# Optimization experiments

Measured on AMD Instinct MI355X. Metric: run time of the kernel, lower is better.

Reference implementation:

```python
import jax, jax.numpy as jnp
import numpy as np

N_NODES = 50000
N_EDGES = 800000
SD = 128
N_GRAPHS = 128
HL = 4
VOCAB = 1340
N_CLASSES = 41
BN_EPS = 1e-5


def setup_inputs() -> dict:
    key = jax.random.key(0)
    ks = jax.random.split(key, 20)
    s = 1.0 / np.sqrt(SD)
    inp = {
        "node_ids": jax.random.randint(ks[0], (N_NODES,), 0, VOCAB),
        "edge_index": jax.random.randint(ks[1], (2, N_EDGES), 0, N_NODES),
        "batch": jnp.sort(jax.random.randint(ks[2], (N_NODES,), 0, N_GRAPHS)),
        "emb": jax.random.normal(ks[3], (VOCAB, SD)) * 0.05,
        "in_W1": jax.random.normal(ks[4], (SD, SD)) * s,
        "in_b1": jnp.zeros((SD,)),
        "in_W2": jax.random.normal(ks[5], (SD, SD)) * s,
        "in_b2": jnp.zeros((SD,)),
        "bn_gamma": jnp.ones((SD,)),
        "bn_beta": jnp.zeros((SD,)),
        "bn_mean": jnp.zeros((SD,)),
        "bn_var": jnp.ones((SD,)),
        "out_W1": jax.random.normal(ks[6], (SD, SD)) * s,
        "out_b1": jnp.zeros((SD,)),
        "out_W2": jax.random.normal(ks[7], (SD, SD)) * s,
        "out_b2": jnp.zeros((SD,)),
        "fc1_W": jax.random.normal(ks[8], (SD, SD)) * s,
        "fc1_b": jnp.zeros((SD,)),
        "fc2_W": jax.random.normal(ks[9], (N_CLASSES, SD)) * s,
        "fc2_b": jnp.zeros((N_CLASSES,)),
    }
    return inp


def reference(node_ids, edge_index, batch, emb, in_W1, in_b1, in_W2, in_b2,
              bn_gamma, bn_beta, bn_mean, bn_var,
              out_W1, out_b1, out_W2, out_b2, fc1_W, fc1_b, fc2_W, fc2_b):
    src, dst = edge_index[0], edge_index[1]

    def gin(x, W1, b1, W2, b2):
        # GINConv with eps=0: mlp(x + sum_{j in N(i)} x_j)
        agg = jax.ops.segment_sum(x[src], dst, num_segments=N_NODES)
        h = x + agg
        h = jnp.maximum(h @ W1.T + b1, 0.0)
        return h @ W2.T + b2

    def bn(x):
        # eval-mode BatchNorm1d with running stats
        return (x - bn_mean) * (bn_gamma / jnp.sqrt(bn_var + BN_EPS)) + bn_beta

    x = emb[node_ids]  # [N, SD]
    x = bn(jnp.maximum(gin(x, in_W1, in_b1, in_W2, in_b2), 0.0))
    for _ in range(HL):  # shared weights, repeated hl times
        x = bn(jnp.maximum(gin(x, in_W1, in_b1, in_W2, in_b2), 0.0))
    x = jnp.maximum(gin(x, out_W1, out_b1, out_W2, out_b2), 0.0)
    pooled = jax.ops.segment_sum(x, batch, num_segments=N_GRAPHS)  # [G, SD]
    h = jnp.maximum(pooled @ fc1_W.T + fc1_b, 0.0)
    return h @ fc2_W.T + fc2_b  # [G, 41]
```

## Files before the change

kernel.cpp:

```cpp
#include <hip/hip_runtime.h>

#define NN 50000
#define NE 800000
#define NG 128
#define NC 41
#define CAP 64
#define XG 8
#define RNG 6250

typedef __attribute__((ext_vector_type(8))) short bfrag8;
typedef __attribute__((ext_vector_type(4))) float facc4;

__device__ __forceinline__ float bf2f(unsigned short u) {
  union { unsigned int i; float f; } v; v.i = ((unsigned int)u) << 16; return v.f;
}
__device__ __forceinline__ unsigned short f2bf(float f) {
  union { float f; unsigned int i; } v; v.f = f;
  unsigned int x = v.i;
  x += 0x7fffu + ((x >> 16) & 1u);
  return (unsigned short)(x >> 16);
}
__device__ __forceinline__ void acc_u4(const uint4 u, float* a) {
  union { unsigned int i; float f; } c;
  c.i = u.x << 16;          a[0] += c.f;
  c.i = u.x & 0xffff0000u;  a[1] += c.f;
  c.i = u.y << 16;          a[2] += c.f;
  c.i = u.y & 0xffff0000u;  a[3] += c.f;
  c.i = u.z << 16;          a[4] += c.f;
  c.i = u.z & 0xffff0000u;  a[5] += c.f;
  c.i = u.w << 16;          a[6] += c.f;
  c.i = u.w & 0xffff0000u;  a[7] += c.f;
}
__device__ __forceinline__ unsigned int pack2(float lo, float hi) {
  return (unsigned int)f2bf(lo) | ((unsigned int)f2bf(hi) << 16);
}

__global__ void prep_kernel(const float* __restrict__ W1, const float* __restrict__ W2,
                            const float* __restrict__ oW1, const float* __restrict__ oW2,
                            const float* __restrict__ gamma, const float* __restrict__ beta,
                            const float* __restrict__ mean, const float* __restrict__ var,
                            unsigned short* W1b, unsigned short* W2b,
                            unsigned short* oW1b, unsigned short* oW2b,
                            float* scale, float* shift) {
  int i = blockIdx.x * 256 + threadIdx.x;
  if (i < 128 * 128) {
    W1b[i] = f2bf(W1[i]);
    W2b[i] = f2bf(W2[i]);
    oW1b[i] = f2bf(oW1[i]);
    oW2b[i] = f2bf(oW2[i]);
  }
  if (i < 128) {
    float s = gamma[i] * rsqrtf(var[i] + 1e-5f);
    scale[i] = s;
    shift[i] = beta[i] - mean[i] * s;
  }
}

__global__ void embed_kernel(const int* __restrict__ node_ids, const float* __restrict__ emb,
                             unsigned short* __restrict__ xb) {
  int idx = blockIdx.x * 256 + threadIdx.x;
  if (idx >= NN * 32) return;
  int node = idx >> 5, f = (idx & 31) * 4;
  const float4 v = *(const float4*)&emb[node_ids[node] * 128 + f];
  ushort4 o;
  o.x = f2bf(v.x); o.y = f2bf(v.y); o.z = f2bf(v.z); o.w = f2bf(v.w);
  *(ushort4*)&xb[node * 128 + f] = o;
}

__global__ __launch_bounds__(256) void fill_kernel(const int* __restrict__ ei,
                                                   int* __restrict__ cnt,
                                                   unsigned short* __restrict__ srclist) {
  int b = blockIdx.x;
  int g = b & 7;
  int s = b >> 3;
  int e = s * 256 + threadIdx.x;
  if (e >= NE) return;
  int d = ei[NE + e];
  unsigned int lo = g * RNG;
  if ((unsigned int)(d - lo) < (unsigned int)RNG) {
    int src = ei[e];
    int pos = atomicAdd(&cnt[d], 1);
    if (pos < CAP) srclist[d * CAP + pos] = (unsigned short)src;
  }
}

__global__ __launch_bounds__(256) void gin_layer_kernel(
    const unsigned short* __restrict__ xin,
    const int* __restrict__ cnt,
    const unsigned short* __restrict__ srclist,
    const unsigned short* __restrict__ W1b,
    const unsigned short* __restrict__ W2b,
    const float* __restrict__ bias1,
    const float* __restrict__ bias2,
    const float* __restrict__ scale,
    const float* __restrict__ shift,
    unsigned short* __restrict__ Out,
    const int* __restrict__ batch,
    float* __restrict__ pooled,
    int M, int mode, int doPool) {
  __shared__ unsigned short sW[128 * 128];
  __shared__ unsigned short sA[64 * 128];
  int tid = threadIdx.x;
  int bRow = blockIdx.x * 64;

  const uint4* gw1 = (const uint4*)W1b;
#pragma unroll
  for (int p = 0; p < 8; ++p) {
    int g = p * 256 + tid;
    int r = g >> 4, b = g & 15;
    int ph = (b + r) & 15;
    *(uint4*)&sW[(r * 16 + ph) * 8] = gw1[g];
  }

  {
    int l16 = tid & 15;
    int sub = tid >> 4;
    int f = l16 * 8;
#pragma unroll 1
    for (int g = 0; g < 4; ++g) {
      int r = g * 16 + sub;
      int node = bRow + r;
      float a[8];
      a[0]=0.f; a[1]=0.f; a[2]=0.f; a[3]=0.f;
      a[4]=0.f; a[5]=0.f; a[6]=0.f; a[7]=0.f;
      if (node < M) {
        acc_u4(*(const uint4*)&xin[node * 128 + f], a);
        int deg = cnt[node];
        if (deg > CAP) deg = CAP;
        const unsigned short* lst = &srclist[node * CAP];
        int j = 0;
        for (; j + 8 <= deg; j += 8) {
          uint4 u0 = *(const uint4*)&xin[(int)lst[j] * 128 + f];
          uint4 u1 = *(const uint4*)&xin[(int)lst[j + 1] * 128 + f];
          uint4 u2 = *(const uint4*)&xin[(int)lst[j + 2] * 128 + f];
          uint4 u3 = *(const uint4*)&xin[(int)lst[j + 3] * 128 + f];
          uint4 u4 = *(const uint4*)&xin[(int)lst[j + 4] * 128 + f];
          uint4 u5 = *(const uint4*)&xin[(int)lst[j + 5] * 128 + f];
          uint4 u6 = *(const uint4*)&xin[(int)lst[j + 6] * 128 + f];
          uint4 u7 = *(const uint4*)&xin[(int)lst[j + 7] * 128 + f];
          acc_u4(u0, a); acc_u4(u1, a); acc_u4(u2, a); acc_u4(u3, a);
          acc_u4(u4, a); acc_u4(u5, a); acc_u4(u6, a); acc_u4(u7, a);
        }
        for (; j + 4 <= deg; j += 4) {
          uint4 u0 = *(const uint4*)&xin[(int)lst[j] * 128 + f];
          uint4 u1 = *(const uint4*)&xin[(int)lst[j + 1] * 128 + f];
          uint4 u2 = *(const uint4*)&xin[(int)lst[j + 2] * 128 + f];
          uint4 u3 = *(const uint4*)&xin[(int)lst[j + 3] * 128 + f];
          acc_u4(u0, a); acc_u4(u1, a); acc_u4(u2, a); acc_u4(u3, a);
        }
        for (; j < deg; ++j) {
          uint4 u = *(const uint4*)&xin[(int)lst[j] * 128 + f];
          acc_u4(u, a);
        }
      }
      int ph = (l16 + r) & 15;
      uint4 o;
      o.x = pack2(a[0], a[1]); o.y = pack2(a[2], a[3]);
      o.z = pack2(a[4], a[5]); o.w = pack2(a[6], a[7]);
      *(uint4*)&sA[(r * 16 + ph) * 8] = o;
    }
  }
  __syncthreads();

  int wave = tid >> 6;
  int lane = tid & 63;
  int l16 = lane & 15;
  int quad = lane >> 4;
  int arow = wave * 16 + l16;

  {
    bfrag8 af[4];
#pragma unroll
    for (int k = 0; k < 4; ++k) {
      int ph = (k * 4 + quad + arow) & 15;
      af[k] = *(const bfrag8*)&sA[(arow * 16 + ph) * 8];
    }
    facc4 acc[8];
#pragma unroll
    for (int t = 0; t < 8; ++t) acc[t] = (facc4){0.f, 0.f, 0.f, 0.f};
#pragma unroll
    for (int k = 0; k < 4; ++k) {
#pragma unroll
      for (int t = 0; t < 8; ++t) {
        int r = t * 16 + l16;
        int ph = (k * 4 + quad + r) & 15;
        bfrag8 bf = *(const bfrag8*)&sW[(r * 16 + ph) * 8];
        acc[t] = __builtin_amdgcn_mfma_f32_16x16x32_bf16(af[k], bf, acc[t], 0, 0, 0);
      }
    }
#pragma unroll
    for (int t = 0; t < 8; ++t) {
      int col = t * 16 + l16;
      float b = bias1[col];
      int cb = col >> 3, ce = col & 7;
#pragma unroll
      for (int i = 0; i < 4; ++i) {
        int row = wave * 16 + quad * 4 + i;
        float v = acc[t][i] + b;
        int ph = (cb + row) & 15;
        sA[(row * 16 + ph) * 8 + ce] = f2bf(v > 0.f ? v : 0.f);
      }
    }
  }
  __syncthreads();

  const uint4* gw2 = (const uint4*)W2b;
#pragma unroll
  for (int p = 0; p < 8; ++p) {
    int g = p * 256 + tid;
    int r = g >> 4, b = g & 15;
    int ph = (b + r) & 15;
    *(uint4*)&sW[(r * 16 + ph) * 8] = gw2[g];
  }
  __syncthreads();

  {
    bfrag8 af[4];
#pragma unroll
    for (int k = 0; k < 4; ++k) {
      int ph = (k * 4 + quad + arow) & 15;
      af[k] = *(const bfrag8*)&sA[(arow * 16 + ph) * 8];
    }
    facc4 acc[8];
#pragma unroll
    for (int t = 0; t < 8; ++t) acc[t] = (facc4){0.f, 0.f, 0.f, 0.f};
#pragma unroll
    for (int k = 0; k < 4; ++k) {
#pragma unroll
      for (int t = 0; t < 8; ++t) {
        int r = t * 16 + l16;
        int ph = (k * 4 + quad + r) & 15;
        bfrag8 bf = *(const bfrag8*)&sW[(r * 16 + ph) * 8];
        acc[t] = __builtin_amdgcn_mfma_f32_16x16x32_bf16(af[k], bf, acc[t], 0, 0, 0);
      }
    }
#pragma unroll
    for (int t = 0; t < 8; ++t) {
      int col = t * 16 + l16;
      float b = bias2[col];
      float sc = 1.f, sh = 0.f;
      if (mode == 1) { sc = scale[col]; sh = shift[col]; }
      int cb = col >> 3, ce = col & 7;
#pragma unroll
      for (int i = 0; i < 4; ++i) {
        int row = wave * 16 + quad * 4 + i;
        float v = acc[t][i] + b;
        v = v > 0.f ? v : 0.f;
        if (mode == 1) v = v * sc + sh;
        int ph = (cb + row) & 15;
        sA[(row * 16 + ph) * 8 + ce] = f2bf(v);
      }
    }
  }
  __syncthreads();

  if (doPool) {
    if (tid < 128) {
      int fcol = tid;
      int cb = fcol >> 3, ce = fcol & 7;
      float acc = 0.f;
      int cur = -1;
      for (int r = 0; r < 64; ++r) {
        int row = bRow + r;
        if (row >= M) break;
        int b = batch[row];
        if (b != cur) {
          if (cur >= 0) atomicAdd(&pooled[cur * 128 + fcol], acc);
          cur = b;
          acc = 0.f;
        }
        int ph = (cb + r) & 15;
        acc += bf2f(sA[(r * 16 + ph) * 8 + ce]);
      }
      if (cur >= 0) atomicAdd(&pooled[cur * 128 + fcol], acc);
    }
  } else {
#pragma unroll
    for (int p = 0; p < 4; ++p) {
      int g = p * 256 + tid;
      int r = g >> 4, b = g & 15;
      int ph = (b + r) & 15;
      int grow = bRow + r;
      if (grow < M)
        *(uint4*)&Out[grow * 128 + b * 8] = *(const uint4*)&sA[(r * 16 + ph) * 8];
    }
  }
}

__global__ __launch_bounds__(128) void fc_kernel(const float* __restrict__ pooled,
                                                 const float* __restrict__ W1,
                                                 const float* __restrict__ b1,
                                                 const float* __restrict__ W2,
                                                 const float* __restrict__ b2,
                                                 float* __restrict__ out) {
  __shared__ float sh1[128];
  __shared__ float sp[128];
  int r = blockIdx.x;
  int c = threadIdx.x;
  sp[c] = pooled[r * 128 + c];
  __syncthreads();
  float acc = 0.f;
  for (int k = 0; k < 128; ++k) acc += sp[k] * W1[c * 128 + k];
  acc += b1[c];
  sh1[c] = acc > 0.f ? acc : 0.f;
  __syncthreads();
  if (c < NC) {
    float o = 0.f;
    for (int k = 0; k < 128; ++k) o += sh1[k] * W2[c * 128 + k];
    out[r * NC + c] = o + b2[c];
  }
}

extern "C" void kernel_launch(void* const* d_in, const int* in_sizes, int n_in,
                              void* d_out, int out_size, void* d_ws, size_t ws_size,
                              hipStream_t stream) {
  const int* node_ids = (const int*)d_in[0];
  const int* edge_index = (const int*)d_in[1];
  const int* batch = (const int*)d_in[2];
  const float* emb = (const float*)d_in[3];
  const float* in_W1 = (const float*)d_in[4];
  const float* in_b1 = (const float*)d_in[5];
  const float* in_W2 = (const float*)d_in[6];
  const float* in_b2 = (const float*)d_in[7];
  const float* bn_gamma = (const float*)d_in[8];
  const float* bn_beta = (const float*)d_in[9];
  const float* bn_mean = (const float*)d_in[10];
  const float* bn_var = (const float*)d_in[11];
  const float* out_W1 = (const float*)d_in[12];
  const float* out_b1 = (const float*)d_in[13];
  const float* out_W2 = (const float*)d_in[14];
  const float* out_b2 = (const float*)d_in[15];
  const float* fc1_W = (const float*)d_in[16];
  const float* fc1_b = (const float*)d_in[17];
  const float* fc2_W = (const float*)d_in[18];
  const float* fc2_b = (const float*)d_in[19];
  float* out = (float*)d_out;

  char* ws = (char*)d_ws;
  size_t off = 0;
  auto alloc = [&](size_t bytes) {
    char* p = ws + off;
    off = (off + bytes + 255) & ~(size_t)255;
    return p;
  };
  unsigned short* xb = (unsigned short*)alloc((size_t)NN * 128 * 2);
  unsigned short* hb = (unsigned short*)alloc((size_t)NN * 128 * 2);
  unsigned short* srclist = (unsigned short*)alloc((size_t)NN * CAP * 2);
  int* cnt = (int*)alloc((size_t)NN * 4);
  unsigned short* W1b = (unsigned short*)alloc(128 * 128 * 2);
  unsigned short* W2b = (unsigned short*)alloc(128 * 128 * 2);
  unsigned short* oW1b = (unsigned short*)alloc(128 * 128 * 2);
  unsigned short* oW2b = (unsigned short*)alloc(128 * 128 * 2);
  float* bnscale = (float*)alloc(128 * 4);
  float* bnshift = (float*)alloc(128 * 4);
  float* pooled = (float*)alloc(NG * 128 * 4);

  hipMemsetAsync(cnt, 0, (size_t)NN * 4, stream);
  hipMemsetAsync(pooled, 0, (size_t)NG * 128 * 4, stream);

  prep_kernel<<<64, 256, 0, stream>>>(in_W1, in_W2, out_W1, out_W2,
                                      bn_gamma, bn_beta, bn_mean, bn_var,
                                      W1b, W2b, oW1b, oW2b, bnscale, bnshift);
  int chunks = (NE + 255) / 256;
  fill_kernel<<<chunks * XG, 256, 0, stream>>>(edge_index, cnt, srclist);
  embed_kernel<<<(NN * 32 + 255) / 256, 256, 0, stream>>>(node_ids, emb, xb);

  int mlp_blocks = (NN + 63) / 64;
  const unsigned short* cur = xb;
  unsigned short* nxt = hb;
  for (int l = 0; l < 6; ++l) {
    const unsigned short* w1 = (l < 5) ? W1b : oW1b;
    const unsigned short* w2 = (l < 5) ? W2b : oW2b;
    const float* b1 = (l < 5) ? in_b1 : out_b1;
    const float* b2 = (l < 5) ? in_b2 : out_b2;
    int mode2 = (l < 5) ? 1 : 0;
    int doPool = (l == 5) ? 1 : 0;
    gin_layer_kernel<<<mlp_blocks, 256, 0, stream>>>(
        cur, cnt, srclist, w1, w2, b1, b2, bnscale, bnshift,
        nxt, batch, pooled, NN, mode2, doPool);
    const unsigned short* t = cur;
    cur = nxt;
    nxt = (unsigned short*)t;
  }

  fc_kernel<<<NG, 128, 0, stream>>>(pooled, fc1_W, fc1_b, fc2_W, fc2_b, out);
}
```

Measured before the change: 482.2 us.

## Read GIN MLP weights from global memory instead of LDS to raise occupancy

Drops the 32 KB shared-memory weight tile. Each wave now loads its MFMA B-fragments for W1 and W2 straight from global memory, and the two block barriers around the W2 reload are gone. It also adds a launch-bounds occupancy hint and loads the neighbor index list 8 or 4 indices at a time with vector loads. The aim is more resident blocks to hide the latency of the memory-bound neighbor gather. The cost is that every wave now re-reads the full weight matrices through the cache hierarchy.

New measurement: 534.3 us. +10.8%, slower.

```diff
diff --git a/kernel.cpp b/kernel.cpp
--- a/kernel.cpp
+++ b/kernel.cpp
@@ -84,7 +84,7 @@
   }
 }
 
-__global__ __launch_bounds__(256) void gin_layer_kernel(
+__global__ __launch_bounds__(256, 5) void gin_layer_kernel(
     const unsigned short* __restrict__ xin,
     const int* __restrict__ cnt,
     const unsigned short* __restrict__ srclist,
@@ -98,24 +98,14 @@
     const int* __restrict__ batch,
     float* __restrict__ pooled,
     int M, int mode, int doPool) {
-  __shared__ unsigned short sW[128 * 128];
   __shared__ unsigned short sA[64 * 128];
   int tid = threadIdx.x;
   int bRow = blockIdx.x * 64;
 
-  const uint4* gw1 = (const uint4*)W1b;
-#pragma unroll
-  for (int p = 0; p < 8; ++p) {
-    int g = p * 256 + tid;
-    int r = g >> 4, b = g & 15;
-    int ph = (b + r) & 15;
-    *(uint4*)&sW[(r * 16 + ph) * 8] = gw1[g];
-  }
-
   {
-    int l16 = tid & 15;
+    int al16 = tid & 15;
     int sub = tid >> 4;
-    int f = l16 * 8;
+    int f = al16 * 8;
 #pragma unroll 1
     for (int g = 0; g < 4; ++g) {
       int r = g * 16 + sub;
@@ -130,22 +120,30 @@
         const unsigned short* lst = &srclist[node * CAP];
         int j = 0;
         for (; j + 8 <= deg; j += 8) {
-          uint4 u0 = *(const uint4*)&xin[(int)lst[j] * 128 + f];
-          uint4 u1 = *(const uint4*)&xin[(int)lst[j + 1] * 128 + f];
-          uint4 u2 = *(const uint4*)&xin[(int)lst[j + 2] * 128 + f];
-          uint4 u3 = *(const uint4*)&xin[(int)lst[j + 3] * 128 + f];
-          uint4 u4 = *(const uint4*)&xin[(int)lst[j + 4] * 128 + f];
-          uint4 u5 = *(const uint4*)&xin[(int)lst[j + 5] * 128 + f];
-          uint4 u6 = *(const uint4*)&xin[(int)lst[j + 6] * 128 + f];
-          uint4 u7 = *(const uint4*)&xin[(int)lst[j + 7] * 128 + f];
+          uint4 iv = *(const uint4*)&lst[j];
+          int n0 = iv.x & 0xffff, n1 = iv.x >> 16;
+          int n2 = iv.y & 0xffff, n3 = iv.y >> 16;
+          int n4 = iv.z & 0xffff, n5 = iv.z >> 16;
+          int n6 = iv.w & 0xffff, n7 = iv.w >> 16;
+          uint4 u0 = *(const uint4*)&xin[n0 * 128 + f];
+          uint4 u1 = *(const uint4*)&xin[n1 * 128 + f];
+          uint4 u2 = *(const uint4*)&xin[n2 * 128 + f];
+          uint4 u3 = *(const uint4*)&xin[n3 * 128 + f];
+          uint4 u4 = *(const uint4*)&xin[n4 * 128 + f];
+          uint4 u5 = *(const uint4*)&xin[n5 * 128 + f];
+          uint4 u6 = *(const uint4*)&xin[n6 * 128 + f];
+          uint4 u7 = *(const uint4*)&xin[n7 * 128 + f];
           acc_u4(u0, a); acc_u4(u1, a); acc_u4(u2, a); acc_u4(u3, a);
           acc_u4(u4, a); acc_u4(u5, a); acc_u4(u6, a); acc_u4(u7, a);
         }
         for (; j + 4 <= deg; j += 4) {
-          uint4 u0 = *(const uint4*)&xin[(int)lst[j] * 128 + f];
-          uint4 u1 = *(const uint4*)&xin[(int)lst[j + 1] * 128 + f];
-          uint4 u2 = *(const uint4*)&xin[(int)lst[j + 2] * 128 + f];
-          uint4 u3 = *(const uint4*)&xin[(int)lst[j + 3] * 128 + f];
+          uint2 iv = *(const uint2*)&lst[j];
+          int n0 = iv.x & 0xffff, n1 = iv.x >> 16;
+          int n2 = iv.y & 0xffff, n3 = iv.y >> 16;
+          uint4 u0 = *(const uint4*)&xin[n0 * 128 + f];
+          uint4 u1 = *(const uint4*)&xin[n1 * 128 + f];
+          uint4 u2 = *(const uint4*)&xin[n2 * 128 + f];
+          uint4 u3 = *(const uint4*)&xin[n3 * 128 + f];
           acc_u4(u0, a); acc_u4(u1, a); acc_u4(u2, a); acc_u4(u3, a);
         }
         for (; j < deg; ++j) {
@@ -153,7 +151,7 @@
           acc_u4(u, a);
         }
       }
-      int ph = (l16 + r) & 15;
+      int ph = (al16 + r) & 15;
       uint4 o;
       o.x = pack2(a[0], a[1]); o.y = pack2(a[2], a[3]);
       o.z = pack2(a[4], a[5]); o.w = pack2(a[6], a[7]);
@@ -168,6 +166,9 @@
   int quad = lane >> 4;
   int arow = wave * 16 + l16;
 
+  const bfrag8* w1f = (const bfrag8*)W1b;
+  const bfrag8* w2f = (const bfrag8*)W2b;
+
   {
     bfrag8 af[4];
 #pragma unroll
@@ -183,8 +184,7 @@
 #pragma unroll
       for (int t = 0; t < 8; ++t) {
         int r = t * 16 + l16;
-        int ph = (k * 4 + quad + r) & 15;
-        bfrag8 bf = *(const bfrag8*)&sW[(r * 16 + ph) * 8];
+        bfrag8 bf = w1f[r * 16 + k * 4 + quad];
         acc[t] = __builtin_amdgcn_mfma_f32_16x16x32_bf16(af[k], bf, acc[t], 0, 0, 0);
       }
     }
@@ -202,17 +202,6 @@
       }
     }
   }
-  __syncthreads();
-
-  const uint4* gw2 = (const uint4*)W2b;
-#pragma unroll
-  for (int p = 0; p < 8; ++p) {
-    int g = p * 256 + tid;
-    int r = g >> 4, b = g & 15;
-    int ph = (b + r) & 15;
-    *(uint4*)&sW[(r * 16 + ph) * 8] = gw2[g];
-  }
-  __syncthreads();
 
   {
     bfrag8 af[4];
@@ -229,8 +218,7 @@
 #pragma unroll
       for (int t = 0; t < 8; ++t) {
         int r = t * 16 + l16;
-        int ph = (k * 4 + quad + r) & 15;
-        bfrag8 bf = *(const bfrag8*)&sW[(r * 16 + ph) * 8];
+        bfrag8 bf = w2f[r * 16 + k * 4 + quad];
         acc[t] = __builtin_amdgcn_mfma_f32_16x16x32_bf16(af[k], bf, acc[t], 0, 0, 0);
       }
     }
```

## Bucket neighbor lists by source chunk and gather chunk-by-chunk for locality

Applied to the files above, without the earlier changes.

The fill kernel splits each destination's neighbor list into 7 buckets keyed by source node range, each with its own counter and capacity of 16. The aggregation loop now iterates over source chunks in the outer loop and over the block's 4 node groups inside, so all threads in a block gather from the same 2MB slice of features at once, aiming to improve L2 hit rate. In exchange, the per-chunk lists are short, so the unrolled path rarely fires and fewer loads are in flight. There is also more counter memory and a small risk of truncation if a chunk exceeds 16 entries.

Result: slower. 910.3 us (+88.8%).

```diff
diff --git a/kernel.cpp b/kernel.cpp
--- a/kernel.cpp
+++ b/kernel.cpp
@@ -4,9 +4,12 @@
 #define NE 800000
 #define NG 128
 #define NC 41
-#define CAP 64
 #define XG 8
 #define RNG 6250
+#define NCH 7
+#define CAPC 16
+#define CSTR (NCH * CAPC)
+#define CNTSTR 8
 
 typedef __attribute__((ext_vector_type(8))) short bfrag8;
 typedef __attribute__((ext_vector_type(4))) float facc4;
@@ -79,8 +82,9 @@
   unsigned int lo = g * RNG;
   if ((unsigned int)(d - lo) < (unsigned int)RNG) {
     int src = ei[e];
-    int pos = atomicAdd(&cnt[d], 1);
-    if (pos < CAP) srclist[d * CAP + pos] = (unsigned short)src;
+    int ch = src >> 13;
+    int pos = atomicAdd(&cnt[d * CNTSTR + ch], 1);
+    if (pos < CAPC) srclist[d * CSTR + ch * CAPC + pos] = (unsigned short)src;
   }
 }
 
@@ -113,50 +117,53 @@
   }
 
   {
-    int l16 = tid & 15;
+    int al16 = tid & 15;
     int sub = tid >> 4;
-    int f = l16 * 8;
+    int f = al16 * 8;
+    float a[4][8];
+#pragma unroll
+    for (int g = 0; g < 4; ++g)
+#pragma unroll
+      for (int q = 0; q < 8; ++q) a[g][q] = 0.f;
+
+#pragma unroll
+    for (int g = 0; g < 4; ++g) {
+      int node = bRow + g * 16 + sub;
+      if (node < M) acc_u4(*(const uint4*)&xin[node * 128 + f], a[g]);
+    }
+
 #pragma unroll 1
+    for (int ch = 0; ch < NCH; ++ch) {
+#pragma unroll
+      for (int g = 0; g < 4; ++g) {
+        int node = bRow + g * 16 + sub;
+        if (node < M) {
+          int d = cnt[node * CNTSTR + ch];
+          if (d > CAPC) d = CAPC;
+          const unsigned short* lst = &srclist[node * CSTR + ch * CAPC];
+          int j = 0;
+          for (; j + 4 <= d; j += 4) {
+            uint4 u0 = *(const uint4*)&xin[(int)lst[j] * 128 + f];
+            uint4 u1 = *(const uint4*)&xin[(int)lst[j + 1] * 128 + f];
+            uint4 u2 = *(const uint4*)&xin[(int)lst[j + 2] * 128 + f];
+            uint4 u3 = *(const uint4*)&xin[(int)lst[j + 3] * 128 + f];
+            acc_u4(u0, a[g]); acc_u4(u1, a[g]); acc_u4(u2, a[g]); acc_u4(u3, a[g]);
+          }
+          for (; j < d; ++j) {
+            uint4 u = *(const uint4*)&xin[(int)lst[j] * 128 + f];
+            acc_u4(u, a[g]);
+          }
+        }
+      }
+    }
+
+#pragma unroll
     for (int g = 0; g < 4; ++g) {
       int r = g * 16 + sub;
-      int node = bRow + r;
-      float a[8];
-      a[0]=0.f; a[1]=0.f; a[2]=0.f; a[3]=0.f;
-      a[4]=0.f; a[5]=0.f; a[6]=0.f; a[7]=0.f;
-      if (node < M) {
-        acc_u4(*(const uint4*)&xin[node * 128 + f], a);
-        int deg = cnt[node];
-        if (deg > CAP) deg = CAP;
-        const unsigned short* lst = &srclist[node * CAP];
-        int j = 0;
-        for (; j + 8 <= deg; j += 8) {
-          uint4 u0 = *(const uint4*)&xin[(int)lst[j] * 128 + f];
-          uint4 u1 = *(const uint4*)&xin[(int)lst[j + 1] * 128 + f];
-          uint4 u2 = *(const uint4*)&xin[(int)lst[j + 2] * 128 + f];
-          uint4 u3 = *(const uint4*)&xin[(int)lst[j + 3] * 128 + f];
-          uint4 u4 = *(const uint4*)&xin[(int)lst[j + 4] * 128 + f];
-          uint4 u5 = *(const uint4*)&xin[(int)lst[j + 5] * 128 + f];
-          uint4 u6 = *(const uint4*)&xin[(int)lst[j + 6] * 128 + f];
-          uint4 u7 = *(const uint4*)&xin[(int)lst[j + 7] * 128 + f];
-          acc_u4(u0, a); acc_u4(u1, a); acc_u4(u2, a); acc_u4(u3, a);
-          acc_u4(u4, a); acc_u4(u5, a); acc_u4(u6, a); acc_u4(u7, a);
-        }
-        for (; j + 4 <= deg; j += 4) {
-          uint4 u0 = *(const uint4*)&xin[(int)lst[j] * 128 + f];
-          uint4 u1 = *(const uint4*)&xin[(int)lst[j + 1] * 128 + f];
-          uint4 u2 = *(const uint4*)&xin[(int)lst[j + 2] * 128 + f];
-          uint4 u3 = *(const uint4*)&xin[(int)lst[j + 3] * 128 + f];
-          acc_u4(u0, a); acc_u4(u1, a); acc_u4(u2, a); acc_u4(u3, a);
-        }
-        for (; j < deg; ++j) {
-          uint4 u = *(const uint4*)&xin[(int)lst[j] * 128 + f];
-          acc_u4(u, a);
-        }
-      }
-      int ph = (l16 + r) & 15;
+      int ph = (al16 + r) & 15;
       uint4 o;
-      o.x = pack2(a[0], a[1]); o.y = pack2(a[2], a[3]);
-      o.z = pack2(a[4], a[5]); o.w = pack2(a[6], a[7]);
+      o.x = pack2(a[g][0], a[g][1]); o.y = pack2(a[g][2], a[g][3]);
+      o.z = pack2(a[g][4], a[g][5]); o.w = pack2(a[g][6], a[g][7]);
       *(uint4*)&sA[(r * 16 + ph) * 8] = o;
     }
   }
@@ -345,8 +352,8 @@
   };
   unsigned short* xb = (unsigned short*)alloc((size_t)NN * 128 * 2);
   unsigned short* hb = (unsigned short*)alloc((size_t)NN * 128 * 2);
-  unsigned short* srclist = (unsigned short*)alloc((size_t)NN * CAP * 2);
-  int* cnt = (int*)alloc((size_t)NN * 4);
+  unsigned short* srclist = (unsigned short*)alloc((size_t)NN * CSTR * 2);
+  int* cnt = (int*)alloc((size_t)NN * CNTSTR * 4);
   unsigned short* W1b = (unsigned short*)alloc(128 * 128 * 2);
   unsigned short* W2b = (unsigned short*)alloc(128 * 128 * 2);
   unsigned short* oW1b = (unsigned short*)alloc(128 * 128 * 2);
@@ -355,7 +362,7 @@
   float* bnshift = (float*)alloc(128 * 4);
   float* pooled = (float*)alloc(NG * 128 * 4);
 
-  hipMemsetAsync(cnt, 0, (size_t)NN * 4, stream);
+  hipMemsetAsync(cnt, 0, (size_t)NN * CNTSTR * 4, stream);
   hipMemsetAsync(pooled, 0, (size_t)NG * 128 * 4, stream);
 
   prep_kernel<<<64, 256, 0, stream>>>(in_W1, in_W2, out_W1, out_W2,
```
